# Performance work log

Measured on AMD Instinct MI355X. Metric: run time of the kernel, lower is better.

The kernel has to match this reference:

```python
import jax, jax.numpy as jnp
import numpy as np

N_HEADS = 16

def setup_inputs() -> dict:
    key = jax.random.key(0)
    k1, k2, k3, k4 = jax.random.split(key, 4)
    B, S, H = 2, 2048, 1024
    x = jax.random.normal(k1, (B, S, H), dtype=jnp.float32)
    pos_table = jax.random.normal(k2, (S, H), dtype=jnp.float32) * 0.02
    W_qkv = jax.random.normal(k3, (H, 3 * H), dtype=jnp.float32) * (1.0 / np.sqrt(H))
    W_out = jax.random.normal(k4, (H, H), dtype=jnp.float32) * (1.0 / np.sqrt(H))
    return {"x": x, "pos_table": pos_table, "W_qkv": W_qkv, "W_out": W_out}


def reference(x, pos_table, W_qkv, W_out):
    B, S, Hd = x.shape
    nh = N_HEADS
    hs = Hd // nh  # head_size
    NEG_INF = jnp.float32(-10000.0)

    pos = pos_table[:S][None, :, :]  # [1, S, H]
    # q, k come from (x + pos_emb); v comes from x alone (duplicate projection)
    qk_proj = (x + pos) @ W_qkv              # [B, S, 3H]
    q = qk_proj[..., :Hd]
    k = qk_proj[..., Hd:2 * Hd]
    v = x @ W_qkv[:, 2 * Hd:]                # [B, S, H]

    def split_heads(t):  # [B, S, H] -> [B, nh, S, hs]
        return t.reshape(B, S, nh, hs).transpose(0, 2, 1, 3)

    q, k, v = split_heads(q), split_heads(k), split_heads(v)

    scores = jnp.einsum('bhqd,bhkd->bhqk', q, k) / jnp.sqrt(jnp.float32(hs))
    q_ind = jnp.arange(S)[:, None]
    k_ind = jnp.arange(S)[None, :]
    mask = q_ind < k_ind  # True where future (masked)
    scores = jnp.where(mask, NEG_INF, scores)

    probs = jax.nn.softmax(scores, axis=-1)
    out = jnp.einsum('bhqk,bhkd->bhqd', probs, v)  # [B, nh, S, hs]
    out = out.transpose(0, 2, 1, 3).reshape(B, S, Hd)
    return out @ W_out
```

## Files before the change

kernel.cpp:

```cpp
#include <hip/hip_runtime.h>

#define SEQ     2048
#define HDIM    1024
#define TOKENS  4096
#define NHEADS  16
#define HS      64
#define LP      72

typedef __bf16 v8bf __attribute__((ext_vector_type(8)));
typedef float  v4f  __attribute__((ext_vector_type(4)));

#define MFMA16(a, b, c) __builtin_amdgcn_mfma_f32_16x16x32_bf16((a), (b), (c), 0, 0, 0)

#define QSCALE (0.125f * 1.44269504088896f)

__device__ __forceinline__ unsigned short f2bf(float f) {
  unsigned int u = __float_as_uint(f);
  u += 0x7FFFu + ((u >> 16) & 1u);
  return (unsigned short)(u >> 16);
}

__device__ __forceinline__ void async16(const void* g, void* l) {
  __builtin_amdgcn_global_load_lds(
      (const __attribute__((address_space(1))) void*)g,
      (__attribute__((address_space(3))) void*)l, 16, 0, 0);
}

__global__ __launch_bounds__(256) void prep_all_kernel(
    const float* __restrict__ x, const float* __restrict__ pos,
    const float* __restrict__ Wqkv, const float* __restrict__ Wout,
    unsigned short* __restrict__ X, unsigned short* __restrict__ XP,
    unsigned short* __restrict__ WQT, unsigned short* __restrict__ WOT) {
  __shared__ float tile[32][33];
  const int id = blockIdx.x;
  if (id < 4096) {
    const int i = (id * 256 + threadIdx.x) * 4;
    float4 xv = *(const float4*)(x + i);
    float4 pv = *(const float4*)(pos + (i & (SEQ * HDIM - 1)));
    ushort4 a, b;
    a.x = f2bf(xv.x); a.y = f2bf(xv.y); a.z = f2bf(xv.z); a.w = f2bf(xv.w);
    b.x = f2bf(xv.x + pv.x); b.y = f2bf(xv.y + pv.y);
    b.z = f2bf(xv.z + pv.z); b.w = f2bf(xv.w + pv.w);
    *(ushort4*)(X + i) = a;
    *(ushort4*)(XP + i) = b;
    return;
  }
  const float* in; unsigned short* out; int R, C, bx, by;
  if (id < 7168) {
    const int t2 = id - 4096;
    in = Wqkv; out = WQT; R = HDIM; C = 3 * HDIM;
    bx = (t2 % 96) * 32; by = (t2 / 96) * 32;
  } else {
    const int t3 = id - 7168;
    in = Wout; out = WOT; R = HDIM; C = HDIM;
    bx = (t3 & 31) * 32; by = (t3 >> 5) * 32;
  }
  const int tx = threadIdx.x & 31, ty = threadIdx.x >> 5;
#pragma unroll
  for (int j = 0; j < 32; j += 8)
    tile[ty + j][tx] = in[(size_t)(by + ty + j) * C + bx + tx];
  __syncthreads();
#pragma unroll
  for (int j = 0; j < 32; j += 8)
    out[(size_t)(bx + ty + j) * R + by + tx] = f2bf(tile[tx][ty + j]);
}

__global__ __launch_bounds__(256) void gemm_qkv_kernel(
    const unsigned short* __restrict__ XP, const unsigned short* __restrict__ X,
    const unsigned short* __restrict__ Wt,
    unsigned short* __restrict__ Qb, unsigned short* __restrict__ Kb,
    unsigned short* __restrict__ VTb) {
  __shared__ unsigned short SM[17408];
  unsigned short* As = SM;
  unsigned short* Bs = SM + 4096;
  const int m0 = blockIdx.x * 128;
  const int n0 = blockIdx.y * 128;
  const unsigned short* A = (n0 < 2 * HDIM) ? XP : X;
  const int t = threadIdx.x;
  const int lane = t & 63, w = t >> 6;
  const int wm = (w >> 1) * 64, wn = (w & 1) * 64;
  const int quad = lane >> 4, l15 = lane & 15;

  v4f acc[4][4] = {};

  const int rowA = t >> 2;
  const int colA = (t & 3) * 8;
  const unsigned short* gA = A + (size_t)(m0 + rowA) * HDIM + colA;
  const unsigned short* gB = Wt + (size_t)(n0 + rowA) * HDIM + colA;
  unsigned short* lA = &As[t * 8];
  unsigned short* lB = &Bs[t * 8];

  for (int k0 = 0; k0 < HDIM; k0 += 32) {
    __syncthreads();
    async16(gA + k0, lA);
    async16(gA + 64 * HDIM + k0, lA + 64 * 32);
    async16(gB + k0, lB);
    async16(gB + 64 * HDIM + k0, lB + 64 * 32);
    __syncthreads();
    v8bf a[4], b[4];
#pragma unroll
    for (int i = 0; i < 4; i++)
      a[i] = *(const v8bf*)&As[(wm + i * 16 + l15) * 32 + quad * 8];
#pragma unroll
    for (int i = 0; i < 4; i++)
      b[i] = *(const v8bf*)&Bs[(wn + i * 16 + l15) * 32 + quad * 8];
#pragma unroll
    for (int i = 0; i < 4; i++)
#pragma unroll
      for (int j = 0; j < 4; j++)
        acc[i][j] = MFMA16(a[i], b[j], acc[i][j]);
  }

  const int b_ = m0 >> 11;
  const int s0 = m0 & (SEQ - 1);

  if (n0 >= 2 * HDIM) {
    unsigned short* St = SM;
    __syncthreads();
#pragma unroll
    for (int i = 0; i < 4; i++)
#pragma unroll
      for (int j = 0; j < 4; j++) {
        ushort4 u;
        u.x = f2bf(acc[i][j][0]); u.y = f2bf(acc[i][j][1]);
        u.z = f2bf(acc[i][j][2]); u.w = f2bf(acc[i][j][3]);
        *(ushort4*)&St[(wn + j * 16 + l15) * 136 + wm + i * 16 + quad * 4] = u;
      }
    __syncthreads();
#pragma unroll
    for (int it = 0; it < 8; it++) {
      const int lin = it * 256 + t;
      const int n = lin >> 4, s8 = (lin & 15) * 8;
      const int c2 = (n0 - 2 * HDIM) + n;
      const int h = c2 >> 6, d = c2 & 63;
      *(uint4*)(VTb + ((size_t)(((b_ << 4) | h) * HS + d)) * SEQ + s0 + s8) =
          *(const uint4*)&St[n * 136 + s8];
    }
  } else {
    const float scale = (n0 < HDIM) ? QSCALE : 1.0f;
    unsigned short* dst = (n0 < HDIM) ? Qb : Kb;
#pragma unroll
    for (int i = 0; i < 4; i++) {
#pragma unroll
      for (int j = 0; j < 4; j++) {
#pragma unroll
        for (int r = 0; r < 4; r++) {
          const int s_ = s0 + wm + i * 16 + quad * 4 + r;
          const int c2 = (n0 & (HDIM - 1)) + wn + j * 16 + l15;
          const int h = c2 >> 6, d = c2 & 63;
          dst[((size_t)(((b_ << 4) | h) * SEQ + s_)) * HS + d] =
              f2bf(acc[i][j][r] * scale);
        }
      }
    }
  }
}

__global__ __launch_bounds__(256, 2) void attn_pair_kernel(
    const unsigned short* __restrict__ Qp, const unsigned short* __restrict__ Kp,
    const unsigned short* __restrict__ Vp, unsigned short* __restrict__ ATTN) {
  __shared__ unsigned short Qs[128 * LP];
  __shared__ unsigned short Ks[64 * LP];
  __shared__ unsigned short Vs[64 * LP];
  __shared__ unsigned short Ps[4][32 * LP];

  const int p  = blockIdx.x;
  const int bh = blockIdx.y;
  const int b_ = bh >> 4, h = bh & 15;
  const int qlo = p, qhi = 31 - p;
  const int q0lo = qlo * 64, q0hi = qhi * 64;
  const int t = threadIdx.x;
  const int lane = t & 63, w = t >> 6;
  const int quad = lane >> 4, l15 = lane & 15;

  const unsigned short* Qg = Qp + (size_t)bh * SEQ * HS;
  const unsigned short* Kg = Kp + (size_t)bh * SEQ * HS;
  const unsigned short* Vg = Vp + (size_t)bh * HS * SEQ;

  const int sr = t >> 3, scol = (t & 7) * 8;
  *(uint4*)&Qs[sr * LP + scol] = *(const uint4*)(Qg + (size_t)(q0lo + sr) * HS + scol);
  *(uint4*)&Qs[(sr + 32) * LP + scol] =
      *(const uint4*)(Qg + (size_t)(q0lo + sr + 32) * HS + scol);
  *(uint4*)&Qs[(sr + 64) * LP + scol] =
      *(const uint4*)(Qg + (size_t)(q0hi + sr) * HS + scol);
  *(uint4*)&Qs[(sr + 96) * LP + scol] =
      *(const uint4*)(Qg + (size_t)(q0hi + sr + 32) * HS + scol);
  __syncthreads();

  v8bf bq[2][2];
#pragma unroll
  for (int tl = 0; tl < 2; tl++)
#pragma unroll
    for (int kh = 0; kh < 2; kh++)
      bq[tl][kh] = *(const v8bf*)&Qs[(tl * 64 + w * 16 + l15) * LP + kh * 32 + quad * 8];

  v8bf ones;
#pragma unroll
  for (int j = 0; j < 8; j++) ones[j] = (__bf16)1.0f;

  v4f o[2][4] = {};
  v4f lacc[2] = {};

  uint4 kr0, kr1, vr0, vr1;
  kr0 = *(const uint4*)(Kg + (size_t)sr * HS + scol);
  kr1 = *(const uint4*)(Kg + (size_t)(sr + 32) * HS + scol);
  vr0 = *(const uint4*)(Vg + (size_t)sr * SEQ + scol);
  vr1 = *(const uint4*)(Vg + (size_t)(sr + 32) * SEQ + scol);

  const int qrow_hi = q0hi + w * 16 + l15;
  const int qrow_lo = q0lo + w * 16 + l15;

  for (int cI = 0; cI <= qhi; cI++) {
    const int kc = cI * 64;
    __syncthreads();
    *(uint4*)&Ks[sr * LP + scol] = kr0;
    *(uint4*)&Ks[(sr + 32) * LP + scol] = kr1;
    *(uint4*)&Vs[sr * LP + scol] = vr0;
    *(uint4*)&Vs[(sr + 32) * LP + scol] = vr1;
    if (cI < qhi) {
      const int kn = kc + 64;
      kr0 = *(const uint4*)(Kg + (size_t)(kn + sr) * HS + scol);
      kr1 = *(const uint4*)(Kg + (size_t)(kn + sr + 32) * HS + scol);
      vr0 = *(const uint4*)(Vg + (size_t)sr * SEQ + kn + scol);
      vr1 = *(const uint4*)(Vg + (size_t)(sr + 32) * SEQ + kn + scol);
    }
    __syncthreads();

    v8bf kf0[4], kf1[4];
#pragma unroll
    for (int ni = 0; ni < 4; ni++) {
      kf0[ni] = *(const v8bf*)&Ks[(ni * 16 + l15) * LP + quad * 8];
      kf1[ni] = *(const v8bf*)&Ks[(ni * 16 + l15) * LP + 32 + quad * 8];
    }

    const bool doLo = (cI <= qlo);

    {
      v4f sc[4] = {};
#pragma unroll
      for (int ni = 0; ni < 4; ni++) {
        sc[ni] = MFMA16(kf0[ni], bq[1][0], sc[ni]);
        sc[ni] = MFMA16(kf1[ni], bq[1][1], sc[ni]);
      }
      if (cI == qhi) {
#pragma unroll
        for (int ni = 0; ni < 4; ni++) {
          const int key = kc + ni * 16 + quad * 4;
#pragma unroll
          for (int r = 0; r < 4; r++)
            if (key + r > qrow_hi) sc[ni][r] = -1e30f;
        }
      }
#pragma unroll
      for (int ni = 0; ni < 4; ni++) {
        const float p0 = exp2f(sc[ni][0]), p1 = exp2f(sc[ni][1]);
        const float p2 = exp2f(sc[ni][2]), p3 = exp2f(sc[ni][3]);
        uint2 pk;
        pk.x = __builtin_amdgcn_perm(__float_as_uint(p1), __float_as_uint(p0), 0x07060302u);
        pk.y = __builtin_amdgcn_perm(__float_as_uint(p3), __float_as_uint(p2), 0x07060302u);
        *(uint2*)&Ps[w][(16 + l15) * LP + ni * 16 + quad * 4] = pk;
      }
    }
    if (doLo) {
      v4f sc[4] = {};
#pragma unroll
      for (int ni = 0; ni < 4; ni++) {
        sc[ni] = MFMA16(kf0[ni], bq[0][0], sc[ni]);
        sc[ni] = MFMA16(kf1[ni], bq[0][1], sc[ni]);
      }
      if (cI == qlo) {
#pragma unroll
        for (int ni = 0; ni < 4; ni++) {
          const int key = kc + ni * 16 + quad * 4;
#pragma unroll
          for (int r = 0; r < 4; r++)
            if (key + r > qrow_lo) sc[ni][r] = -1e30f;
        }
      }
#pragma unroll
      for (int ni = 0; ni < 4; ni++) {
        const float p0 = exp2f(sc[ni][0]), p1 = exp2f(sc[ni][1]);
        const float p2 = exp2f(sc[ni][2]), p3 = exp2f(sc[ni][3]);
        uint2 pk;
        pk.x = __builtin_amdgcn_perm(__float_as_uint(p1), __float_as_uint(p0), 0x07060302u);
        pk.y = __builtin_amdgcn_perm(__float_as_uint(p3), __float_as_uint(p2), 0x07060302u);
        *(uint2*)&Ps[w][l15 * LP + ni * 16 + quad * 4] = pk;
      }
    }

#pragma unroll
    for (int ki = 0; ki < 2; ki++) {
      v8bf pahi = *(const v8bf*)&Ps[w][(16 + l15) * LP + ki * 32 + quad * 8];
      lacc[1] = MFMA16(pahi, ones, lacc[1]);
      v8bf palo;
      if (doLo) {
        palo = *(const v8bf*)&Ps[w][l15 * LP + ki * 32 + quad * 8];
        lacc[0] = MFMA16(palo, ones, lacc[0]);
      }
#pragma unroll
      for (int ni = 0; ni < 4; ni++) {
        v8bf vb = *(const v8bf*)&Vs[(ni * 16 + l15) * LP + ki * 32 + quad * 8];
        o[1][ni] = MFMA16(pahi, vb, o[1][ni]);
        if (doLo) o[0][ni] = MFMA16(palo, vb, o[0][ni]);
      }
    }
  }

#pragma unroll
  for (int tl = 0; tl < 2; tl++) {
    const int q0 = tl ? q0hi : q0lo;
    const int row_base = q0 + w * 16 + quad * 4;
    float invl[4];
#pragma unroll
    for (int r = 0; r < 4; r++) invl[r] = 1.0f / lacc[tl][r];
#pragma unroll
    for (int ni = 0; ni < 4; ni++)
#pragma unroll
      for (int r = 0; r < 4; r++) {
        const int tr = b_ * SEQ + row_base + r;
        ATTN[(size_t)tr * HDIM + h * HS + ni * 16 + l15] = f2bf(o[tl][ni][r] * invl[r]);
      }
  }
}

__global__ __launch_bounds__(256) void gemm_out_kernel(
    const unsigned short* __restrict__ Ab, const unsigned short* __restrict__ Wt,
    float* __restrict__ out) {
  __shared__ unsigned short As[128 * 32];
  __shared__ unsigned short Bs[128 * 32];
  const int m0 = blockIdx.x * 128;
  const int n0 = blockIdx.y * 128;
  const int t = threadIdx.x;
  const int lane = t & 63, w = t >> 6;
  const int wm = (w >> 1) * 64, wn = (w & 1) * 64;
  const int quad = lane >> 4, l15 = lane & 15;

  v4f acc[4][4] = {};

  const int rowA = t >> 2;
  const int colA = (t & 3) * 8;
  const unsigned short* gA = Ab + (size_t)(m0 + rowA) * HDIM + colA;
  const unsigned short* gB = Wt + (size_t)(n0 + rowA) * HDIM + colA;
  unsigned short* lA = &As[t * 8];
  unsigned short* lB = &Bs[t * 8];

  for (int k0 = 0; k0 < HDIM; k0 += 32) {
    __syncthreads();
    async16(gA + k0, lA);
    async16(gA + 64 * HDIM + k0, lA + 64 * 32);
    async16(gB + k0, lB);
    async16(gB + 64 * HDIM + k0, lB + 64 * 32);
    __syncthreads();
    v8bf a[4], b[4];
#pragma unroll
    for (int i = 0; i < 4; i++)
      a[i] = *(const v8bf*)&As[(wm + i * 16 + l15) * 32 + quad * 8];
#pragma unroll
    for (int i = 0; i < 4; i++)
      b[i] = *(const v8bf*)&Bs[(wn + i * 16 + l15) * 32 + quad * 8];
#pragma unroll
    for (int i = 0; i < 4; i++)
#pragma unroll
      for (int j = 0; j < 4; j++)
        acc[i][j] = MFMA16(a[i], b[j], acc[i][j]);
  }

#pragma unroll
  for (int i = 0; i < 4; i++) {
#pragma unroll
    for (int j = 0; j < 4; j++) {
#pragma unroll
      for (int r = 0; r < 4; r++) {
        const int tr = m0 + wm + i * 16 + quad * 4 + r;
        const int c = n0 + wn + j * 16 + l15;
        out[(size_t)tr * HDIM + c] = acc[i][j][r];
      }
    }
  }
}

extern "C" void kernel_launch(void* const* d_in, const int* in_sizes, int n_in,
                              void* d_out, int out_size, void* d_ws, size_t ws_size,
                              hipStream_t stream) {
  (void)in_sizes; (void)n_in; (void)out_size; (void)ws_size;
  const float* x    = (const float*)d_in[0];
  const float* pos  = (const float*)d_in[1];
  const float* Wqkv = (const float*)d_in[2];
  const float* Wout = (const float*)d_in[3];
  float* out = (float*)d_out;

  char* ws = (char*)d_ws;
  unsigned short* XP   = (unsigned short*)(ws);
  unsigned short* X    = (unsigned short*)(ws + ((size_t)8  << 20));
  unsigned short* WQT  = (unsigned short*)(ws + ((size_t)16 << 20));
  unsigned short* WOT  = (unsigned short*)(ws + ((size_t)22 << 20));
  unsigned short* Qb   = (unsigned short*)(ws + ((size_t)24 << 20));
  unsigned short* Kb   = (unsigned short*)(ws + ((size_t)32 << 20));
  unsigned short* VTb  = (unsigned short*)(ws + ((size_t)40 << 20));
  unsigned short* ATTN = (unsigned short*)(ws + ((size_t)48 << 20));

  prep_all_kernel<<<8192, 256, 0, stream>>>(x, pos, Wqkv, Wout, X, XP, WQT, WOT);

  dim3 g1(TOKENS / 128, 3 * HDIM / 128);
  gemm_qkv_kernel<<<g1, 256, 0, stream>>>(XP, X, WQT, Qb, Kb, VTb);

  dim3 g2(16, 2 * NHEADS);
  attn_pair_kernel<<<g2, 256, 0, stream>>>(Qb, Kb, VTb, ATTN);

  dim3 g3(TOKENS / 128, HDIM / 128);
  gemm_out_kernel<<<g3, 256, 0, stream>>>(ATTN, WOT, out);
}
```

Measured before the change: 198.7 us.

## Split attention key range across two blocks and merge partials in combine kernel

The attention kernel now splits each query-pair's key chunks between two blocks (even/odd chunks), writing unnormalized bf16 partial outputs and row sums that a new combine kernel adds and normalizes. This doubles the attention grid to improve occupancy and load balance, and shared memory is reduced by aliasing Q and P buffers so more blocks fit per CU. The V-transpose epilogue in the QKV GEMM drops its LDS staging and writes scattered 8-byte stores directly. The change adds an extra kernel launch, partial-result traffic, and a bf16 rounding of partials before summation.

Result: slower. 268.9 us (+35.3%).

```diff
diff --git a/kernel.cpp b/kernel.cpp
--- a/kernel.cpp
+++ b/kernel.cpp
@@ -18,6 +18,9 @@
   unsigned int u = __float_as_uint(f);
   u += 0x7FFFu + ((u >> 16) & 1u);
   return (unsigned short)(u >> 16);
+}
+__device__ __forceinline__ float bf2f(unsigned short u) {
+  return __uint_as_float((unsigned int)u << 16);
 }
 
 __device__ __forceinline__ void async16(const void* g, void* l) {
@@ -70,9 +73,8 @@
     const unsigned short* __restrict__ Wt,
     unsigned short* __restrict__ Qb, unsigned short* __restrict__ Kb,
     unsigned short* __restrict__ VTb) {
-  __shared__ unsigned short SM[17408];
-  unsigned short* As = SM;
-  unsigned short* Bs = SM + 4096;
+  __shared__ unsigned short As[128 * 32];
+  __shared__ unsigned short Bs[128 * 32];
   const int m0 = blockIdx.x * 128;
   const int n0 = blockIdx.y * 128;
   const unsigned short* A = (n0 < 2 * HDIM) ? XP : X;
@@ -115,26 +117,18 @@
   const int s0 = m0 & (SEQ - 1);
 
   if (n0 >= 2 * HDIM) {
-    unsigned short* St = SM;
-    __syncthreads();
-#pragma unroll
-    for (int i = 0; i < 4; i++)
+#pragma unroll
+    for (int i = 0; i < 4; i++) {
 #pragma unroll
       for (int j = 0; j < 4; j++) {
+        const int c2 = (n0 - 2 * HDIM) + wn + j * 16 + l15;
+        const int h = c2 >> 6, d = c2 & 63;
+        const int s_ = s0 + wm + i * 16 + quad * 4;
         ushort4 u;
         u.x = f2bf(acc[i][j][0]); u.y = f2bf(acc[i][j][1]);
         u.z = f2bf(acc[i][j][2]); u.w = f2bf(acc[i][j][3]);
-        *(ushort4*)&St[(wn + j * 16 + l15) * 136 + wm + i * 16 + quad * 4] = u;
-      }
-    __syncthreads();
-#pragma unroll
-    for (int it = 0; it < 8; it++) {
-      const int lin = it * 256 + t;
-      const int n = lin >> 4, s8 = (lin & 15) * 8;
-      const int c2 = (n0 - 2 * HDIM) + n;
-      const int h = c2 >> 6, d = c2 & 63;
-      *(uint4*)(VTb + ((size_t)(((b_ << 4) | h) * HS + d)) * SEQ + s0 + s8) =
-          *(const uint4*)&St[n * 136 + s8];
+        *(ushort4*)(VTb + ((size_t)(((b_ << 4) | h) * HS + d)) * SEQ + s_) = u;
+      }
     }
   } else {
     const float scale = (n0 < HDIM) ? QSCALE : 1.0f;
@@ -156,17 +150,18 @@
   }
 }
 
-__global__ __launch_bounds__(256, 2) void attn_pair_kernel(
+__global__ __launch_bounds__(256, 4) void attn_kernel(
     const unsigned short* __restrict__ Qp, const unsigned short* __restrict__ Kp,
-    const unsigned short* __restrict__ Vp, unsigned short* __restrict__ ATTN) {
-  __shared__ unsigned short Qs[128 * LP];
-  __shared__ unsigned short Ks[64 * LP];
-  __shared__ unsigned short Vs[64 * LP];
-  __shared__ unsigned short Ps[4][32 * LP];
-
-  const int p  = blockIdx.x;
+    const unsigned short* __restrict__ Vp,
+    unsigned short* __restrict__ PART_O, float* __restrict__ PART_L) {
+  __shared__ unsigned short SM[18432];
+  unsigned short* Ks = SM;
+  unsigned short* Vs = SM + 4608;
+  unsigned short* QPs = SM + 9216;
+
+  const int p  = blockIdx.x >> 1;
+  const int sg = blockIdx.x & 1;
   const int bh = blockIdx.y;
-  const int b_ = bh >> 4, h = bh & 15;
   const int qlo = p, qhi = 31 - p;
   const int q0lo = qlo * 64, q0hi = qhi * 64;
   const int t = threadIdx.x;
@@ -178,12 +173,12 @@
   const unsigned short* Vg = Vp + (size_t)bh * HS * SEQ;
 
   const int sr = t >> 3, scol = (t & 7) * 8;
-  *(uint4*)&Qs[sr * LP + scol] = *(const uint4*)(Qg + (size_t)(q0lo + sr) * HS + scol);
-  *(uint4*)&Qs[(sr + 32) * LP + scol] =
+  *(uint4*)&QPs[sr * LP + scol] = *(const uint4*)(Qg + (size_t)(q0lo + sr) * HS + scol);
+  *(uint4*)&QPs[(sr + 32) * LP + scol] =
       *(const uint4*)(Qg + (size_t)(q0lo + sr + 32) * HS + scol);
-  *(uint4*)&Qs[(sr + 64) * LP + scol] =
+  *(uint4*)&QPs[(sr + 64) * LP + scol] =
       *(const uint4*)(Qg + (size_t)(q0hi + sr) * HS + scol);
-  *(uint4*)&Qs[(sr + 96) * LP + scol] =
+  *(uint4*)&QPs[(sr + 96) * LP + scol] =
       *(const uint4*)(Qg + (size_t)(q0hi + sr + 32) * HS + scol);
   __syncthreads();
 
@@ -192,7 +187,9 @@
   for (int tl = 0; tl < 2; tl++)
 #pragma unroll
     for (int kh = 0; kh < 2; kh++)
-      bq[tl][kh] = *(const v8bf*)&Qs[(tl * 64 + w * 16 + l15) * LP + kh * 32 + quad * 8];
+      bq[tl][kh] = *(const v8bf*)&QPs[(tl * 64 + w * 16 + l15) * LP + kh * 32 + quad * 8];
+
+  unsigned short* Ps_w = QPs + w * 32 * LP;
 
   v8bf ones;
 #pragma unroll
@@ -202,23 +199,26 @@
   v4f lacc[2] = {};
 
   uint4 kr0, kr1, vr0, vr1;
-  kr0 = *(const uint4*)(Kg + (size_t)sr * HS + scol);
-  kr1 = *(const uint4*)(Kg + (size_t)(sr + 32) * HS + scol);
-  vr0 = *(const uint4*)(Vg + (size_t)sr * SEQ + scol);
-  vr1 = *(const uint4*)(Vg + (size_t)(sr + 32) * SEQ + scol);
+  {
+    const int kc = sg * 64;
+    kr0 = *(const uint4*)(Kg + (size_t)(kc + sr) * HS + scol);
+    kr1 = *(const uint4*)(Kg + (size_t)(kc + sr + 32) * HS + scol);
+    vr0 = *(const uint4*)(Vg + (size_t)sr * SEQ + kc + scol);
+    vr1 = *(const uint4*)(Vg + (size_t)(sr + 32) * SEQ + kc + scol);
+  }
 
   const int qrow_hi = q0hi + w * 16 + l15;
   const int qrow_lo = q0lo + w * 16 + l15;
 
-  for (int cI = 0; cI <= qhi; cI++) {
+  for (int cI = sg; cI <= qhi; cI += 2) {
     const int kc = cI * 64;
     __syncthreads();
     *(uint4*)&Ks[sr * LP + scol] = kr0;
     *(uint4*)&Ks[(sr + 32) * LP + scol] = kr1;
     *(uint4*)&Vs[sr * LP + scol] = vr0;
     *(uint4*)&Vs[(sr + 32) * LP + scol] = vr1;
-    if (cI < qhi) {
-      const int kn = kc + 64;
+    if (cI + 2 <= qhi) {
+      const int kn = kc + 128;
       kr0 = *(const uint4*)(Kg + (size_t)(kn + sr) * HS + scol);
       kr1 = *(const uint4*)(Kg + (size_t)(kn + sr + 32) * HS + scol);
       vr0 = *(const uint4*)(Vg + (size_t)sr * SEQ + kn + scol);
@@ -258,7 +258,7 @@
         uint2 pk;
         pk.x = __builtin_amdgcn_perm(__float_as_uint(p1), __float_as_uint(p0), 0x07060302u);
         pk.y = __builtin_amdgcn_perm(__float_as_uint(p3), __float_as_uint(p2), 0x07060302u);
-        *(uint2*)&Ps[w][(16 + l15) * LP + ni * 16 + quad * 4] = pk;
+        *(uint2*)&Ps_w[(16 + l15) * LP + ni * 16 + quad * 4] = pk;
       }
     }
     if (doLo) {
@@ -284,17 +284,17 @@
         uint2 pk;
         pk.x = __builtin_amdgcn_perm(__float_as_uint(p1), __float_as_uint(p0), 0x07060302u);
         pk.y = __builtin_amdgcn_perm(__float_as_uint(p3), __float_as_uint(p2), 0x07060302u);
-        *(uint2*)&Ps[w][l15 * LP + ni * 16 + quad * 4] = pk;
+        *(uint2*)&Ps_w[l15 * LP + ni * 16 + quad * 4] = pk;
       }
     }
 
 #pragma unroll
     for (int ki = 0; ki < 2; ki++) {
-      v8bf pahi = *(const v8bf*)&Ps[w][(16 + l15) * LP + ki * 32 + quad * 8];
+      v8bf pahi = *(const v8bf*)&Ps_w[(16 + l15) * LP + ki * 32 + quad * 8];
       lacc[1] = MFMA16(pahi, ones, lacc[1]);
       v8bf palo;
       if (doLo) {
-        palo = *(const v8bf*)&Ps[w][l15 * LP + ki * 32 + quad * 8];
+        palo = *(const v8bf*)&Ps_w[l15 * LP + ki * 32 + quad * 8];
         lacc[0] = MFMA16(palo, ones, lacc[0]);
       }
 #pragma unroll
@@ -308,19 +308,73 @@
 
 #pragma unroll
   for (int tl = 0; tl < 2; tl++) {
-    const int q0 = tl ? q0hi : q0lo;
-    const int row_base = q0 + w * 16 + quad * 4;
-    float invl[4];
-#pragma unroll
-    for (int r = 0; r < 4; r++) invl[r] = 1.0f / lacc[tl][r];
+    const int slot = (((bh * 16 + p) * 2 + tl) * 2) + sg;
+    unsigned short* po = PART_O + (size_t)slot * 4096;
+    const int rb = w * 16 + quad * 4;
 #pragma unroll
     for (int ni = 0; ni < 4; ni++)
 #pragma unroll
-      for (int r = 0; r < 4; r++) {
-        const int tr = b_ * SEQ + row_base + r;
-        ATTN[(size_t)tr * HDIM + h * HS + ni * 16 + l15] = f2bf(o[tl][ni][r] * invl[r]);
-      }
-  }
+      for (int r = 0; r < 4; r++)
+        po[(rb + r) * 64 + ni * 16 + l15] = f2bf(o[tl][ni][r]);
+    if (l15 == 0) {
+      float* pl = PART_L + (size_t)slot * 64;
+#pragma unroll
+      for (int r = 0; r < 4; r++) pl[rb + r] = lacc[tl][r];
+    }
+  }
+}
+
+__global__ __launch_bounds__(256) void combine_kernel(
+    const unsigned short* __restrict__ PART_O, const float* __restrict__ PART_L,
+    unsigned short* __restrict__ ATTN) {
+  const int q = blockIdx.x;
+  const int bh = blockIdx.y;
+  const int b_ = bh >> 4, h = bh & 15;
+  const int p = min(q, 31 - q);
+  const int tl = (q >= 16) ? 1 : 0;
+  const int base = ((bh * 16 + p) * 2 + tl) * 2;
+  const int t = threadIdx.x;
+  const int row = t >> 2, c0 = (t & 3) * 16;
+
+  const float Lsum = PART_L[(size_t)base * 64 + row] +
+                     PART_L[(size_t)(base + 1) * 64 + row];
+  const float inv = 1.0f / Lsum;
+
+  float acc[16];
+#pragma unroll
+  for (int j = 0; j < 16; j++) acc[j] = 0.0f;
+#pragma unroll
+  for (int s = 0; s < 2; s++) {
+    const unsigned short* po = PART_O + (size_t)(base + s) * 4096 + row * 64 + c0;
+    ushort4 u0 = *(const ushort4*)(po);
+    ushort4 u1 = *(const ushort4*)(po + 4);
+    ushort4 u2 = *(const ushort4*)(po + 8);
+    ushort4 u3 = *(const ushort4*)(po + 12);
+    acc[0]  += bf2f(u0.x); acc[1]  += bf2f(u0.y);
+    acc[2]  += bf2f(u0.z); acc[3]  += bf2f(u0.w);
+    acc[4]  += bf2f(u1.x); acc[5]  += bf2f(u1.y);
+    acc[6]  += bf2f(u1.z); acc[7]  += bf2f(u1.w);
+    acc[8]  += bf2f(u2.x); acc[9]  += bf2f(u2.y);
+    acc[10] += bf2f(u2.z); acc[11] += bf2f(u2.w);
+    acc[12] += bf2f(u3.x); acc[13] += bf2f(u3.y);
+    acc[14] += bf2f(u3.z); acc[15] += bf2f(u3.w);
+  }
+
+  const int tr = b_ * SEQ + q * 64 + row;
+  unsigned short* dst = ATTN + (size_t)tr * HDIM + h * HS + c0;
+  ushort4 o0, o1, o2, o3;
+  o0.x = f2bf(acc[0] * inv);  o0.y = f2bf(acc[1] * inv);
+  o0.z = f2bf(acc[2] * inv);  o0.w = f2bf(acc[3] * inv);
+  o1.x = f2bf(acc[4] * inv);  o1.y = f2bf(acc[5] * inv);
+  o1.z = f2bf(acc[6] * inv);  o1.w = f2bf(acc[7] * inv);
+  o2.x = f2bf(acc[8] * inv);  o2.y = f2bf(acc[9] * inv);
+  o2.z = f2bf(acc[10] * inv); o2.w = f2bf(acc[11] * inv);
+  o3.x = f2bf(acc[12] * inv); o3.y = f2bf(acc[13] * inv);
+  o3.z = f2bf(acc[14] * inv); o3.w = f2bf(acc[15] * inv);
+  *(ushort4*)(dst) = o0;
+  *(ushort4*)(dst + 4) = o1;
+  *(ushort4*)(dst + 8) = o2;
+  *(ushort4*)(dst + 12) = o3;
 }
 
 __global__ __launch_bounds__(256) void gemm_out_kernel(
@@ -398,14 +452,19 @@
   unsigned short* Kb   = (unsigned short*)(ws + ((size_t)32 << 20));
   unsigned short* VTb  = (unsigned short*)(ws + ((size_t)40 << 20));
   unsigned short* ATTN = (unsigned short*)(ws + ((size_t)48 << 20));
+  unsigned short* PART_O = (unsigned short*)(ws);
+  float*          PART_L = (float*)(ws + ((size_t)18 << 20));
 
   prep_all_kernel<<<8192, 256, 0, stream>>>(x, pos, Wqkv, Wout, X, XP, WQT, WOT);
 
   dim3 g1(TOKENS / 128, 3 * HDIM / 128);
   gemm_qkv_kernel<<<g1, 256, 0, stream>>>(XP, X, WQT, Qb, Kb, VTb);
 
-  dim3 g2(16, 2 * NHEADS);
-  attn_pair_kernel<<<g2, 256, 0, stream>>>(Qb, Kb, VTb, ATTN);
+  dim3 g2(32, 2 * NHEADS);
+  attn_kernel<<<g2, 256, 0, stream>>>(Qb, Kb, VTb, PART_O, PART_L);
+
+  dim3 gc(32, 2 * NHEADS);
+  combine_kernel<<<gc, 256, 0, stream>>>(PART_O, PART_L, ATTN);
 
   dim3 g3(TOKENS / 128, HDIM / 128);
   gemm_out_kernel<<<g3, 256, 0, stream>>>(ATTN, WOT, out);
```
